# Kernel tuning notes

Hardware: AMD Instinct MI355X
Metric: run time of the kernel (lower is better)

Reference implementation:

```python
import jax, jax.numpy as jnp
import numpy as np
import math

B, N, H, NH, HD, G = 2, 1024, 512, 8, 64, 50
MAX_DIST = 10.0


def setup_inputs() -> dict:
    key = jax.random.key(0)
    ks = jax.random.split(key, 12)
    s = 0.02  # small init scale for weights
    return {
        'x': jax.random.normal(ks[0], (B, N, H), jnp.float32),
        'distances': jax.random.uniform(ks[1], (B, N, N), jnp.float32) * MAX_DIST,
        'mask': jnp.ones((B, N), jnp.int32),
        'widths': jnp.ones((G,), jnp.float32) * 0.5,
        'dp_w': jax.random.normal(ks[2], (G, NH), jnp.float32) * s,
        'dp_b': jnp.zeros((NH,), jnp.float32),
        'wq': jax.random.normal(ks[3], (H, H), jnp.float32) * s,
        'bq': jnp.zeros((H,), jnp.float32),
        'wk': jax.random.normal(ks[4], (H, H), jnp.float32) * s,
        'bk': jnp.zeros((H,), jnp.float32),
        'wv': jax.random.normal(ks[5], (H, H), jnp.float32) * s,
        'bv': jnp.zeros((H,), jnp.float32),
        'wo': jax.random.normal(ks[6], (H, H), jnp.float32) * s,
        'bo': jnp.zeros((H,), jnp.float32),
        'ln1_g': jnp.ones((H,), jnp.float32),
        'ln1_b': jnp.zeros((H,), jnp.float32),
        'ln2_g': jnp.ones((H,), jnp.float32),
        'ln2_b': jnp.zeros((H,), jnp.float32),
        'w1': jax.random.normal(ks[7], (H, 4 * H), jnp.float32) * s,
        'b1': jnp.zeros((4 * H,), jnp.float32),
        'w2': jax.random.normal(ks[8], (4 * H, H), jnp.float32) * s,
        'b2': jnp.zeros((H,), jnp.float32),
    }


def _layernorm(x, g, b, eps=1e-5):
    mu = jnp.mean(x, axis=-1, keepdims=True)
    var = jnp.mean(jnp.square(x - mu), axis=-1, keepdims=True)
    return (x - mu) * jax.lax.rsqrt(var + eps) * g + b


def reference(x, distances, mask, widths, dp_w, dp_b, wq, bq, wk, bk, wv, bv,
              wo, bo, ln1_g, ln1_b, ln2_g, ln2_b, w1, b1, w2, b2):
    centers = jnp.linspace(0.0, MAX_DIST, G, dtype=jnp.float32)  # buffer

    residual = x
    xn = _layernorm(x, ln1_g, ln1_b)

    def split_heads(t):  # [B,N,H] -> [B,NH,N,HD]
        return t.reshape(B, N, NH, HD).transpose(0, 2, 1, 3)

    q = split_heads(xn @ wq + bq)
    k = split_heads(xn @ wk + bk)
    v = split_heads(xn @ wv + bv)

    scores = jnp.einsum('bhqd,bhkd->bhqk', q, k) / math.sqrt(HD)

    # Gaussian distance encoding: [B,N,N,G]
    diff = distances[..., None] - centers
    gf = jnp.exp(-jnp.square(diff) / (2.0 * jnp.square(widths)))
    # project to per-head bias, then permute to [B,NH,N,N]
    dist_bias = (gf @ dp_w + dp_b).transpose(0, 3, 1, 2)
    scores = scores + dist_bias

    key_mask = mask[:, None, None, :]  # [B,1,1,N]
    scores = jnp.where(key_mask == 0, -1e9, scores)

    attn = jax.nn.softmax(scores, axis=-1)
    out = jnp.einsum('bhqk,bhkd->bhqd', attn, v)
    out = out.transpose(0, 2, 1, 3).reshape(B, N, H)
    out = out @ wo + bo

    x = residual + out
    residual = x
    xn = _layernorm(x, ln2_g, ln2_b)
    h = jax.nn.gelu(xn @ w1 + b1, approximate=False)  # dropout is identity in eval
    x = residual + (h @ w2 + b2)
    return x
```

## Files before the change

### kernel.cpp

```cpp
#include <hip/hip_runtime.h>
#include <hip/hip_bf16.h>
#include <math.h>

#define B_ 2
#define N_ 1024
#define H_ 512
#define NH_ 8
#define HD_ 64
#define G_ 50
#define TAB_ 1024
constexpr float MAXD = 10.0f;

typedef __attribute__((ext_vector_type(8))) short short8;
typedef __attribute__((ext_vector_type(4))) float f32x4;

__device__ inline ushort f2bf(float v) {
  __hip_bfloat16 h = __float2bfloat16(v);
  return *(ushort*)&h;
}
__device__ inline float bf2f(ushort u) {
  unsigned x = ((unsigned)u) << 16;
  return __uint_as_float(x);
}
__device__ inline void gload_lds16(const ushort* g, ushort* l) {
  __builtin_amdgcn_global_load_lds(
      (const __attribute__((address_space(1))) void*)g,
      (__attribute__((address_space(3))) void*)l, 16, 0, 0);
}

__device__ inline void transp_dev(const float* __restrict__ src,
                                  ushort* __restrict__ d, int R, int C,
                                  int bx, int by, int t, float (*tile)[33]) {
  int r0 = by * 32, c0 = bx * 32;
  int rr = t >> 5, cc = t & 31;
  #pragma unroll
  for (int p = 0; p < 4; ++p)
    tile[rr + p * 8][cc] = src[(size_t)(r0 + rr + p * 8) * C + c0 + cc];
  __syncthreads();
  #pragma unroll
  for (int p = 0; p < 4; ++p)
    d[(size_t)(c0 + rr + p * 8) * R + r0 + cc] = f2bf(tile[cc][rr + p * 8]);
}

__global__ __launch_bounds__(256) void prep_k(
    const float* wq, const float* wk, const float* wv, const float* wo,
    const float* w1, const float* w2, ushort* __restrict__ wT4,
    ushort* __restrict__ w1T, ushort* __restrict__ w2T,
    const float* __restrict__ widths, const float* __restrict__ dp_w,
    const float* __restrict__ dp_b, float2* __restrict__ tab2,
    const float* __restrict__ x, const float* __restrict__ ln1g,
    const float* __restrict__ ln1b, ushort* __restrict__ xn) {
  __shared__ float tile[32][33];
  __shared__ float red2[4][2];
  int bid = blockIdx.x, t = threadIdx.x;
  if (bid < 1024) {
    int z = bid >> 8, rem = bid & 255;
    const float* src = (z == 0) ? wq : (z == 1) ? wk : (z == 2) ? wv : wo;
    transp_dev(src, wT4 + (size_t)z * 512 * 512, 512, 512, rem & 15, rem >> 4, t, tile);
  } else if (bid < 2048) {
    int rem = bid - 1024;
    transp_dev(w1, w1T, 512, 2048, rem & 63, rem >> 6, t, tile);
  } else if (bid < 3072) {
    int rem = bid - 2048;
    transp_dev(w2, w2T, 2048, 512, rem & 15, rem >> 4, t, tile);
  } else if (bid < 3105) {
    int i = (bid - 3072) * 256 + t;
    if (i >= NH_ * (TAB_ + 1)) return;
    int h = i / (TAB_ + 1), tt = i % (TAB_ + 1);
    int t1 = tt < TAB_ ? tt + 1 : tt;
    float d0 = (float)tt * (MAXD / TAB_);
    float d1 = (float)t1 * (MAXD / TAB_);
    float v0 = dp_b[h], v1 = dp_b[h];
    for (int g = 0; g < G_; ++g) {
      float c = (float)g * (MAXD / 49.0f);
      float w = widths[g];
      float inv = -1.0f / (2.0f * w * w);
      float wg = dp_w[g * NH_ + h];
      float e0 = d0 - c, e1 = d1 - c;
      v0 += expf(e0 * e0 * inv) * wg;
      v1 += expf(e1 * e1 * inv) * wg;
    }
    tab2[i] = make_float2(v0, v1);
  } else {
    int row = (bid - 3105) * 2 + (t >> 7);
    int tl = t & 127;
    float4 v = *(const float4*)(x + (size_t)row * H_ + tl * 4);
    float s = v.x + v.y + v.z + v.w;
    float sq = v.x * v.x + v.y * v.y + v.z * v.z + v.w * v.w;
    #pragma unroll
    for (int m = 1; m < 64; m <<= 1) {
      s += __shfl_xor(s, m, 64);
      sq += __shfl_xor(sq, m, 64);
    }
    int wid = t >> 6;
    if ((t & 63) == 0) { red2[wid][0] = s; red2[wid][1] = sq; }
    __syncthreads();
    int rw = (t >> 7) * 2;
    s = red2[rw][0] + red2[rw + 1][0];
    sq = red2[rw][1] + red2[rw + 1][1];
    float mu = s * (1.0f / H_);
    float var = sq * (1.0f / H_) - mu * mu;
    float rs = rsqrtf(var + 1e-5f);
    float4 gg = *(const float4*)(ln1g + tl * 4);
    float4 bb = *(const float4*)(ln1b + tl * 4);
    ushort4 o;
    o.x = f2bf((v.x - mu) * rs * gg.x + bb.x);
    o.y = f2bf((v.y - mu) * rs * gg.y + bb.y);
    o.z = f2bf((v.z - mu) * rs * gg.z + bb.z);
    o.w = f2bf((v.w - mu) * rs * gg.w + bb.w);
    *(ushort4*)(xn + (size_t)row * H_ + tl * 4) = o;
  }
}

enum { EPI_QKV = 1, EPI_RES = 2, EPI_GELU = 3, EPI_PART = 4 };

template <int BM, int BN, int EPI>
__global__ __launch_bounds__(256) void mfma_gemm(const ushort* __restrict__ A,
                                                 const ushort* __restrict__ Bt,
                                                 const float* __restrict__ b0,
                                                 const float* __restrict__ b1,
                                                 const float* __restrict__ b2,
                                                 const float* __restrict__ resid,
                                                 void* __restrict__ outv,
                                                 int K, int Ks, int Nc) {
  __shared__ ushort As[2][BM * 32];
  __shared__ ushort Bs[2][BN * 32];
  int t = threadIdx.x;
  int z = blockIdx.z;
  const ushort* Bz;
  int k0;
  if constexpr (EPI == EPI_PART) {
    Bz = Bt;
    k0 = z * K;
  } else {
    Bz = Bt + (size_t)z * Nc * Ks;
    k0 = 0;
  }
  const float* bias = (z == 0) ? b0 : (z == 1) ? b1 : b2;
  int m0 = blockIdx.y * BM, n0 = blockIdx.x * BN;
  int lane = t & 63, w = t >> 6, wr = w >> 1, wc = w & 1;
  int lrow = lane & 15, lkg = lane >> 4;
  constexpr int NFM = BM / 32, NFN = BN / 32;
  constexpr int AL = BM / 64, BL = BN / 64;
  f32x4 acc[NFM][NFN] = {};
  int rl = lane >> 2, kgl = lane & 3;

  auto stage = [&](int buf, int kt) {
    #pragma unroll
    for (int p = 0; p < AL; ++p) {
      int r = w * (BM / 4) + p * 16 + rl;
      int kgs = kgl ^ (r & 3);
      gload_lds16(&A[(size_t)(m0 + r) * Ks + k0 + kt + kgs * 8],
                  &As[buf][(w * (BM / 4) + p * 16) * 32]);
    }
    #pragma unroll
    for (int p = 0; p < BL; ++p) {
      int r = w * (BN / 4) + p * 16 + rl;
      int kgs = kgl ^ (r & 3);
      gload_lds16(&Bz[(size_t)(n0 + r) * Ks + k0 + kt + kgs * 8],
                  &Bs[buf][(w * (BN / 4) + p * 16) * 32]);
    }
  };
  auto compute = [&](int buf) {
    short8 af[NFM], bfr[NFN];
    #pragma unroll
    for (int fm = 0; fm < NFM; ++fm) {
      int r = wr * (BM / 2) + fm * 16 + lrow;
      af[fm] = *(const short8*)&As[buf][r * 32 + ((lkg ^ (r & 3)) << 3)];
    }
    #pragma unroll
    for (int fn = 0; fn < NFN; ++fn) {
      int r = wc * (BN / 2) + fn * 16 + lrow;
      bfr[fn] = *(const short8*)&Bs[buf][r * 32 + ((lkg ^ (r & 3)) << 3)];
    }
    #pragma unroll
    for (int fm = 0; fm < NFM; ++fm)
      #pragma unroll
      for (int fn = 0; fn < NFN; ++fn)
        acc[fm][fn] = __builtin_amdgcn_mfma_f32_16x16x32_bf16(af[fm], bfr[fn],
                                                              acc[fm][fn], 0, 0, 0);
  };

  stage(0, 0);
  __syncthreads();
  int cur = 0;
  for (int kt = 0; kt < K; kt += 32) {
    if (kt + 32 < K) stage(cur ^ 1, kt + 32);
    compute(cur);
    __syncthreads();
    cur ^= 1;
  }

  int rbase = (lane >> 4) * 4;
  #pragma unroll
  for (int fm = 0; fm < NFM; ++fm) {
    #pragma unroll
    for (int fn = 0; fn < NFN; ++fn) {
      #pragma unroll
      for (int j = 0; j < 4; ++j) {
        int row = m0 + wr * (BM / 2) + fm * 16 + rbase + j;
        int col = n0 + wc * (BN / 2) + fn * 16 + lrow;
        if constexpr (EPI == EPI_PART) {
          size_t M = (size_t)gridDim.y * BM;
          ((float*)outv)[(size_t)z * M * Nc + (size_t)row * Nc + col] =
              acc[fm][fn][j];
        } else {
          float v = acc[fm][fn][j] + bias[col];
          if constexpr (EPI == EPI_QKV) {
            ushort* q = (ushort*)outv + (size_t)z * (1 << 20);
            int bb = row >> 10, n = row & (N_ - 1);
            int h = col >> 6, d = col & 63;
            if (z < 2)
              q[(((size_t)(bb * NH_ + h)) * N_ + n) * HD_ + d] = f2bf(v);
            else
              q[(((size_t)(bb * NH_ + h)) * HD_ + d) * N_ + n] = f2bf(v);
          } else if constexpr (EPI == EPI_RES) {
            ((float*)outv)[(size_t)row * Nc + col] =
                resid[(size_t)row * Nc + col] + v;
          } else {
            ((ushort*)outv)[(size_t)row * Nc + col] =
                f2bf(0.5f * v * (1.0f + erff(v * 0.70710678118654752f)));
          }
        }
      }
    }
  }
}

__global__ __launch_bounds__(256) void comb2_k(const float* __restrict__ p,
                                               const float* __restrict__ resid,
                                               const float* __restrict__ bias,
                                               float* __restrict__ out) {
  int idx = blockIdx.x * 256 + threadIdx.x;
  int base = idx * 4;
  int col = base & (H_ - 1);
  f32x4 a = *(const f32x4*)&p[base];
  f32x4 b = *(const f32x4*)&p[(1 << 20) + base];
  f32x4 r = *(const f32x4*)&resid[base];
  f32x4 bi = *(const f32x4*)&bias[col];
  f32x4 o = r + a + b + bi;
  *(f32x4*)&out[base] = o;
}

__global__ __launch_bounds__(128) void comb2ln_k(const float* __restrict__ p,
                                                 const float* __restrict__ resid,
                                                 const float* __restrict__ bias,
                                                 const float* __restrict__ g,
                                                 const float* __restrict__ bl,
                                                 float* __restrict__ x1out,
                                                 ushort* __restrict__ xnout) {
  int row = blockIdx.x, t = threadIdx.x;
  int base = row * H_ + t * 4;
  f32x4 a = *(const f32x4*)&p[base];
  f32x4 b2v = *(const f32x4*)&p[(1 << 20) + base];
  f32x4 r = *(const f32x4*)&resid[base];
  f32x4 bi = *(const f32x4*)&bias[t * 4];
  f32x4 v = r + a + b2v + bi;
  *(f32x4*)&x1out[base] = v;
  float s = v[0] + v[1] + v[2] + v[3];
  float sq = v[0] * v[0] + v[1] * v[1] + v[2] * v[2] + v[3] * v[3];
  #pragma unroll
  for (int m = 1; m < 64; m <<= 1) {
    s += __shfl_xor(s, m, 64);
    sq += __shfl_xor(sq, m, 64);
  }
  __shared__ float red[2][2];
  int wid = t >> 6;
  if ((t & 63) == 0) { red[wid][0] = s; red[wid][1] = sq; }
  __syncthreads();
  s = red[0][0] + red[1][0];
  sq = red[0][1] + red[1][1];
  float mu = s * (1.0f / H_);
  float var = sq * (1.0f / H_) - mu * mu;
  float rs = rsqrtf(var + 1e-5f);
  float4 gg = *(const float4*)(g + t * 4);
  float4 bb = *(const float4*)(bl + t * 4);
  ushort4 o;
  o.x = f2bf((v[0] - mu) * rs * gg.x + bb.x);
  o.y = f2bf((v[1] - mu) * rs * gg.y + bb.y);
  o.z = f2bf((v[2] - mu) * rs * gg.z + bb.z);
  o.w = f2bf((v[3] - mu) * rs * gg.w + bb.w);
  *(ushort4*)(xnout + (size_t)row * H_ + t * 4) = o;
}

constexpr int QT = 64, KT = 64, NJH = 2, NTH = N_ / (KT * NJH);
constexpr int JH = N_ / NJH;

__global__ __launch_bounds__(256) void attn_k(
    const ushort* __restrict__ q, const ushort* __restrict__ k,
    const ushort* __restrict__ v, const float* __restrict__ dist,
    const int* __restrict__ mask, const float2* __restrict__ tab2g,
    float* __restrict__ Op, float2* __restrict__ ml) {
  int qt = blockIdx.x, h = blockIdx.y, z = blockIdx.z;
  int b = z >> 1, jh = z & 1;
  int i0 = qt * QT;
  int jbase = jh * JH;
  __shared__ ushort Ks[2][KT * 64];
  __shared__ ushort Vt[2][64 * KT];
  __shared__ ushort Bsb[2][QT * 68];
  __shared__ ushort Ps[4][16 * 64];
  __shared__ float2 tl2[TAB_ + 1];
  __shared__ float mfl[JH];
  int t = threadIdx.x;
  int lane = t & 63, w = t >> 6;
  int l = lane & 15, g = lane >> 4;

  for (int i = t; i <= TAB_; i += 256) tl2[i] = tab2g[h * (TAB_ + 1) + i];
  for (int i = t; i < JH; i += 256) mfl[i] = (mask[b * N_ + jbase + i] == 0) ? -1e9f : 0.0f;

  const size_t ho = ((size_t)(b * NH_ + h)) * N_ * HD_;
  const ushort* qb = q + ho;
  const ushort* kb = k + ho;
  const ushort* vb = v + ho;

  int qrow = i0 + w * 16 + l;
  short8 qf[2];
  qf[0] = *(const short8*)&qb[(size_t)qrow * 64 + g * 8];
  qf[1] = *(const short8*)&qb[(size_t)qrow * 64 + 32 + g * 8];

  int c2 = t & 7, jr = t >> 3;
  int dr_r = t >> 2, dr_c = (t & 3) * 16;

  auto stK = [&](int buf, short8 val, int j2) {
    *(short8*)&Ks[buf][j2 * 64 + ((c2 ^ (j2 & 7)) << 3)] = val;
  };
  auto stV = [&](int buf, short8 val, int d) {
    *(short8*)&Vt[buf][d * 64 + ((c2 ^ (d & 7)) << 3)] = val;
  };

  short8 k0a, k1a, v0a, v1a;
  f32x4 dda[4];
  {
    const ushort* kn = kb + (size_t)jbase * 64;
    const ushort* vn = vb + jbase;
    k0a = *(const short8*)&kn[(size_t)jr * 64 + c2 * 8];
    k1a = *(const short8*)&kn[(size_t)(jr + 32) * 64 + c2 * 8];
    v0a = *(const short8*)&vn[(size_t)jr * N_ + c2 * 8];
    v1a = *(const short8*)&vn[(size_t)(jr + 32) * N_ + c2 * 8];
    const float* db = dist + ((size_t)b * N_ + (i0 + dr_r)) * N_ + jbase + dr_c;
    #pragma unroll
    for (int p = 0; p < 4; ++p) dda[p] = *(const f32x4*)&db[p * 4];
  }
  __syncthreads();
  {
    stK(0, k0a, jr); stK(0, k1a, jr + 32);
    stV(0, v0a, jr); stV(0, v1a, jr + 32);
    #pragma unroll
    for (int p = 0; p < 4; ++p) {
      ushort4 ov;
      #pragma unroll
      for (int e = 0; e < 4; ++e) {
        int jcol = dr_c + p * 4 + e;
        float u = dda[p][e] * ((float)TAB_ / MAXD);
        int it = (int)u;
        it = it < 0 ? 0 : (it > TAB_ - 1 ? TAB_ - 1 : it);
        float f = u - (float)it;
        float2 tv = tl2[it];
        ((ushort*)&ov)[e] = f2bf(tv.x + f * (tv.y - tv.x) + mfl[jcol]);
      }
      *(ushort4*)&Bsb[0][dr_r * 68 + dr_c + p * 4] = ov;
    }
  }
  __syncthreads();

  float m_[4] = {-1e30f, -1e30f, -1e30f, -1e30f};
  float l_[4] = {0.f, 0.f, 0.f, 0.f};
  f32x4 acc[4] = {{0,0,0,0},{0,0,0,0},{0,0,0,0},{0,0,0,0}};

  int cur = 0;
  for (int tt = 0; tt < NTH; ++tt) {
    const int j0 = jbase + tt * KT;
    if (tt + 1 < NTH) {
      const ushort* kn = kb + (size_t)(j0 + KT) * 64;
      const ushort* vn = vb + (j0 + KT);
      k0a = *(const short8*)&kn[(size_t)jr * 64 + c2 * 8];
      k1a = *(const short8*)&kn[(size_t)(jr + 32) * 64 + c2 * 8];
      v0a = *(const short8*)&vn[(size_t)jr * N_ + c2 * 8];
      v1a = *(const short8*)&vn[(size_t)(jr + 32) * N_ + c2 * 8];
      const float* db = dist + ((size_t)b * N_ + (i0 + dr_r)) * N_ + j0 + KT + dr_c;
      #pragma unroll
      for (int p = 0; p < 4; ++p) dda[p] = *(const f32x4*)&db[p * 4];
    }
    f32x4 sa[4] = {{0,0,0,0},{0,0,0,0},{0,0,0,0},{0,0,0,0}};
    __builtin_amdgcn_s_setprio(1);
    #pragma unroll
    for (int dblk = 0; dblk < 2; ++dblk)
      #pragma unroll
      for (int fj = 0; fj < 4; ++fj) {
        int j2 = fj * 16 + l;
        short8 kf = *(const short8*)&Ks[cur][j2 * 64 + (((dblk * 4 + g) ^ (j2 & 7)) << 3)];
        sa[fj] = __builtin_amdgcn_mfma_f32_16x16x32_bf16(qf[dblk], kf, sa[fj], 0, 0, 0);
      }
    __builtin_amdgcn_s_setprio(0);
    float al_[4];
    int qloc = w * 16 + 4 * g;
    #pragma unroll
    for (int reg = 0; reg < 4; ++reg) {
      float svr[4];
      #pragma unroll
      for (int fj = 0; fj < 4; ++fj)
        svr[fj] = fmaf(sa[fj][reg], 0.125f,
                       bf2f(Bsb[cur][(qloc + reg) * 68 + fj * 16 + l]));
      float rm = fmaxf(fmaxf(svr[0], svr[1]), fmaxf(svr[2], svr[3]));
      rm = fmaxf(rm, __shfl_xor(rm, 1, 64));
      rm = fmaxf(rm, __shfl_xor(rm, 2, 64));
      rm = fmaxf(rm, __shfl_xor(rm, 4, 64));
      rm = fmaxf(rm, __shfl_xor(rm, 8, 64));
      float mn = fmaxf(m_[reg], rm);
      float al = __expf(m_[reg] - mn);
      m_[reg] = mn;
      al_[reg] = al;
      float ps = 0.f;
      int qlq = 4 * g + reg;
      #pragma unroll
      for (int fj = 0; fj < 4; ++fj) {
        float p = __expf(svr[fj] - mn);
        ps += p;
        int c = fj * 2 + (l >> 3);
        Ps[w][qlq * 64 + ((c ^ (qlq & 7)) << 3) + (l & 7)] = f2bf(p);
      }
      ps += __shfl_xor(ps, 1, 64);
      ps += __shfl_xor(ps, 2, 64);
      ps += __shfl_xor(ps, 4, 64);
      ps += __shfl_xor(ps, 8, 64);
      l_[reg] = l_[reg] * al + ps;
    }
    #pragma unroll
    for (int fd = 0; fd < 4; ++fd)
      #pragma unroll
      for (int reg = 0; reg < 4; ++reg) acc[fd][reg] *= al_[reg];
    __builtin_amdgcn_s_setprio(1);
    #pragma unroll
    for (int jj = 0; jj < 2; ++jj) {
      short8 pa = *(const short8*)&Ps[w][l * 64 + (((jj * 4 + g) ^ (l & 7)) << 3)];
      #pragma unroll
      for (int fd = 0; fd < 4; ++fd) {
        int d2 = fd * 16 + l;
        short8 vf = *(const short8*)&Vt[cur][d2 * 64 + (((jj * 4 + g) ^ (d2 & 7)) << 3)];
        acc[fd] = __builtin_amdgcn_mfma_f32_16x16x32_bf16(pa, vf, acc[fd], 0, 0, 0);
      }
    }
    __builtin_amdgcn_s_setprio(0);
    if (tt + 1 < NTH) {
      int nb = cur ^ 1;
      stK(nb, k0a, jr); stK(nb, k1a, jr + 32);
      stV(nb, v0a, jr); stV(nb, v1a, jr + 32);
      const int jloc = (tt + 1) * KT;
      #pragma unroll
      for (int p = 0; p < 4; ++p) {
        ushort4 ov;
        #pragma unroll
        for (int e = 0; e < 4; ++e) {
          int jcol = dr_c + p * 4 + e;
          float u = dda[p][e] * ((float)TAB_ / MAXD);
          int it = (int)u;
          it = it < 0 ? 0 : (it > TAB_ - 1 ? TAB_ - 1 : it);
          float f = u - (float)it;
          float2 tv = tl2[it];
          ((ushort*)&ov)[e] = f2bf(tv.x + f * (tv.y - tv.x) + mfl[jloc + jcol]);
        }
        *(ushort4*)&Bsb[nb][dr_r * 68 + dr_c + p * 4] = ov;
      }
    }
    __syncthreads();
    cur ^= 1;
  }
  const size_t pbase = (((size_t)(b * NJH + jh) * NH_ + h) * N_) + i0;
  #pragma unroll
  for (int reg = 0; reg < 4; ++reg) {
    int rowl = w * 16 + 4 * g + reg;
    float* op = Op + (pbase + rowl) * HD_ + l;
    #pragma unroll
    for (int fd = 0; fd < 4; ++fd) op[fd * 16] = acc[fd][reg];
    if (l == 0) ml[pbase + rowl] = make_float2(m_[reg], l_[reg]);
  }
}

__global__ __launch_bounds__(256) void comb_k(const float* __restrict__ Op,
                                              const float2* __restrict__ ml,
                                              ushort* __restrict__ ao) {
  int idx = blockIdx.x * 256 + threadIdx.x;
  int row = idx >> 4;
  int dq = (idx & 15) * 4;
  int b = row >> 13, h = (row >> 10) & 7, n = row & 1023;
  size_t p0 = (((size_t)(b * NJH + 0) * NH_ + h) * N_) + n;
  size_t p1 = (((size_t)(b * NJH + 1) * NH_ + h) * N_) + n;
  float2 v0 = ml[p0], v1 = ml[p1];
  float M = fmaxf(v0.x, v1.x);
  float a0 = __expf(v0.x - M), a1 = __expf(v1.x - M);
  float inv = 1.0f / (v0.y * a0 + v1.y * a1);
  float4 O0 = *(const float4*)&Op[p0 * HD_ + dq];
  float4 O1 = *(const float4*)&Op[p1 * HD_ + dq];
  ushort4 o;
  o.x = f2bf((O0.x * a0 + O1.x * a1) * inv);
  o.y = f2bf((O0.y * a0 + O1.y * a1) * inv);
  o.z = f2bf((O0.z * a0 + O1.z * a1) * inv);
  o.w = f2bf((O0.w * a0 + O1.w * a1) * inv);
  *(ushort4*)&ao[((size_t)(b * N_ + n)) * H_ + h * HD_ + dq] = o;
}

extern "C" void kernel_launch(void* const* d_in, const int* in_sizes, int n_in,
                              void* d_out, int out_size, void* d_ws, size_t ws_size,
                              hipStream_t stream) {
  const float* x = (const float*)d_in[0];
  const float* distances = (const float*)d_in[1];
  const int* mask = (const int*)d_in[2];
  const float* widths = (const float*)d_in[3];
  const float* dp_w = (const float*)d_in[4];
  const float* dp_b = (const float*)d_in[5];
  const float* wq = (const float*)d_in[6];
  const float* bq = (const float*)d_in[7];
  const float* wk = (const float*)d_in[8];
  const float* bk = (const float*)d_in[9];
  const float* wv = (const float*)d_in[10];
  const float* bv = (const float*)d_in[11];
  const float* wo = (const float*)d_in[12];
  const float* bo = (const float*)d_in[13];
  const float* ln1_g = (const float*)d_in[14];
  const float* ln1_b = (const float*)d_in[15];
  const float* ln2_g = (const float*)d_in[16];
  const float* ln2_b = (const float*)d_in[17];
  const float* w1 = (const float*)d_in[18];
  const float* b1 = (const float*)d_in[19];
  const float* w2 = (const float*)d_in[20];
  const float* b2 = (const float*)d_in[21];
  float* out = (float*)d_out;
  float* wsf = (float*)d_ws;

  const size_t M1 = (size_t)1 << 20;
  ushort* qkvb = (ushort*)wsf;
  float* x1 = wsf + 2 * M1;
  ushort* hbuf = (ushort*)(wsf + 3 * M1);
  ushort* xn = (ushort*)(wsf + 5 * M1);
  ushort* xn2 = (ushort*)(wsf + 5 * M1 + M1 / 2);
  ushort* ao = (ushort*)(wsf + 6 * M1);
  ushort* wT4 = (ushort*)(wsf + 6 * M1 + M1 / 2);
  ushort* w1T = (ushort*)(wsf + 7 * M1);
  ushort* w2T = (ushort*)(wsf + 7 * M1 + M1 / 2);
  float2* tab2 = (float2*)(wsf + 8 * M1);
  float* Op = wsf + 9 * M1;
  float2* ml = (float2*)(wsf + 11 * M1);
  float* pAO = wsf + 12 * M1;
  float* pF2 = wsf + 14 * M1;

  prep_k<<<4129, 256, 0, stream>>>(wq, wk, wv, wo, w1, w2, wT4, w1T, w2T,
                                   widths, dp_w, dp_b, tab2, x, ln1_g, ln1_b, xn);

  mfma_gemm<64, 64, EPI_QKV><<<dim3(8, 32, 3), 256, 0, stream>>>(
      xn, wT4, bq, bk, bv, nullptr, qkvb, 512, 512, 512);

  attn_k<<<dim3(N_ / QT, NH_, B_ * NJH), 256, 0, stream>>>(
      qkvb, qkvb + M1, qkvb + 2 * M1, distances, mask, tab2, Op, ml);
  comb_k<<<1024, 256, 0, stream>>>(Op, ml, ao);

  mfma_gemm<64, 64, EPI_PART><<<dim3(8, 32, 2), 256, 0, stream>>>(
      ao, wT4 + (size_t)3 * 512 * 512, bo, bo, bo, nullptr, pAO, 256, 512, 512);
  comb2ln_k<<<B_ * N_, 128, 0, stream>>>(pAO, x, bo, ln2_g, ln2_b, x1, xn2);

  mfma_gemm<128, 64, EPI_GELU><<<dim3(32, 16, 1), 256, 0, stream>>>(
      xn2, w1T, b1, b1, b1, nullptr, hbuf, 512, 512, 2048);

  mfma_gemm<64, 64, EPI_PART><<<dim3(8, 32, 2), 256, 0, stream>>>(
      hbuf, w2T, b2, b2, b2, nullptr, pF2, 1024, 2048, 512);
  comb2_k<<<1024, 256, 0, stream>>>(pF2, x1, b2, out);
}
```

Measured before the change: 103.5 us.

## Reduce split-K partials inside a 512-thread block and fuse FFN2 residual epilogue

```diff
diff --git a/kernel.cpp b/kernel.cpp
--- a/kernel.cpp
+++ b/kernel.cpp
@@ -127,15 +127,7 @@
   __shared__ ushort Bs[2][BN * 32];
   int t = threadIdx.x;
   int z = blockIdx.z;
-  const ushort* Bz;
-  int k0;
-  if constexpr (EPI == EPI_PART) {
-    Bz = Bt;
-    k0 = z * K;
-  } else {
-    Bz = Bt + (size_t)z * Nc * Ks;
-    k0 = 0;
-  }
+  const ushort* Bz = Bt + (size_t)z * Nc * Ks;
   const float* bias = (z == 0) ? b0 : (z == 1) ? b1 : b2;
   int m0 = blockIdx.y * BM, n0 = blockIdx.x * BN;
   int lane = t & 63, w = t >> 6, wr = w >> 1, wc = w & 1;
@@ -150,14 +142,14 @@
     for (int p = 0; p < AL; ++p) {
       int r = w * (BM / 4) + p * 16 + rl;
       int kgs = kgl ^ (r & 3);
-      gload_lds16(&A[(size_t)(m0 + r) * Ks + k0 + kt + kgs * 8],
+      gload_lds16(&A[(size_t)(m0 + r) * Ks + kt + kgs * 8],
                   &As[buf][(w * (BM / 4) + p * 16) * 32]);
     }
     #pragma unroll
     for (int p = 0; p < BL; ++p) {
       int r = w * (BN / 4) + p * 16 + rl;
       int kgs = kgl ^ (r & 3);
-      gload_lds16(&Bz[(size_t)(n0 + r) * Ks + k0 + kt + kgs * 8],
+      gload_lds16(&Bz[(size_t)(n0 + r) * Ks + kt + kgs * 8],
                   &Bs[buf][(w * (BN / 4) + p * 16) * 32]);
     }
   };
@@ -200,46 +192,119 @@
       for (int j = 0; j < 4; ++j) {
         int row = m0 + wr * (BM / 2) + fm * 16 + rbase + j;
         int col = n0 + wc * (BN / 2) + fn * 16 + lrow;
-        if constexpr (EPI == EPI_PART) {
-          size_t M = (size_t)gridDim.y * BM;
-          ((float*)outv)[(size_t)z * M * Nc + (size_t)row * Nc + col] =
-              acc[fm][fn][j];
+        float v = acc[fm][fn][j] + bias[col];
+        if constexpr (EPI == EPI_QKV) {
+          ushort* q = (ushort*)outv + (size_t)z * (1 << 20);
+          int bb = row >> 10, n = row & (N_ - 1);
+          int h = col >> 6, d = col & 63;
+          if (z < 2)
+            q[(((size_t)(bb * NH_ + h)) * N_ + n) * HD_ + d] = f2bf(v);
+          else
+            q[(((size_t)(bb * NH_ + h)) * HD_ + d) * N_ + n] = f2bf(v);
+        } else if constexpr (EPI == EPI_RES) {
+          ((float*)outv)[(size_t)row * Nc + col] =
+              resid[(size_t)row * Nc + col] + v;
         } else {
-          float v = acc[fm][fn][j] + bias[col];
-          if constexpr (EPI == EPI_QKV) {
-            ushort* q = (ushort*)outv + (size_t)z * (1 << 20);
-            int bb = row >> 10, n = row & (N_ - 1);
-            int h = col >> 6, d = col & 63;
-            if (z < 2)
-              q[(((size_t)(bb * NH_ + h)) * N_ + n) * HD_ + d] = f2bf(v);
-            else
-              q[(((size_t)(bb * NH_ + h)) * HD_ + d) * N_ + n] = f2bf(v);
-          } else if constexpr (EPI == EPI_RES) {
+          ((ushort*)outv)[(size_t)row * Nc + col] =
+              f2bf(0.5f * v * (1.0f + erff(v * 0.70710678118654752f)));
+        }
+      }
+    }
+  }
+}
+
+template <int EPI>
+__global__ __launch_bounds__(512) void mfma_gemm2(const ushort* __restrict__ A,
+                                                  const ushort* __restrict__ Bt,
+                                                  const float* __restrict__ bias,
+                                                  const float* __restrict__ resid,
+                                                  void* __restrict__ outv,
+                                                  int K, int Ks, int Nc) {
+  constexpr int BM = 64, BN = 64;
+  __shared__ ushort AsBs[2][2][2][BM * 32];
+  int t = threadIdx.x;
+  int half = t >> 8;
+  int lane = t & 63;
+  int wl = (t >> 6) & 3;
+  int wr = wl >> 1, wc = wl & 1;
+  int lrow = lane & 15, lkg = lane >> 4;
+  int k0 = half * K;
+  int m0 = blockIdx.y * BM, n0 = blockIdx.x * BN;
+  f32x4 acc[2][2] = {};
+  int rl = lane >> 2, kgl = lane & 3;
+
+  auto stage = [&](int buf, int kt) {
+    int r = wl * 16 + rl;
+    int kgs = kgl ^ (r & 3);
+    gload_lds16(&A[(size_t)(m0 + r) * Ks + k0 + kt + kgs * 8],
+                &AsBs[0][half][buf][(wl * 16) * 32]);
+    gload_lds16(&Bt[(size_t)(n0 + r) * Ks + k0 + kt + kgs * 8],
+                &AsBs[1][half][buf][(wl * 16) * 32]);
+  };
+  auto compute = [&](int buf) {
+    short8 af[2], bfr[2];
+    #pragma unroll
+    for (int fm = 0; fm < 2; ++fm) {
+      int r = wr * 32 + fm * 16 + lrow;
+      af[fm] = *(const short8*)&AsBs[0][half][buf][r * 32 + ((lkg ^ (r & 3)) << 3)];
+    }
+    #pragma unroll
+    for (int fn = 0; fn < 2; ++fn) {
+      int r = wc * 32 + fn * 16 + lrow;
+      bfr[fn] = *(const short8*)&AsBs[1][half][buf][r * 32 + ((lkg ^ (r & 3)) << 3)];
+    }
+    #pragma unroll
+    for (int fm = 0; fm < 2; ++fm)
+      #pragma unroll
+      for (int fn = 0; fn < 2; ++fn)
+        acc[fm][fn] = __builtin_amdgcn_mfma_f32_16x16x32_bf16(af[fm], bfr[fn],
+                                                              acc[fm][fn], 0, 0, 0);
+  };
+
+  stage(0, 0);
+  __syncthreads();
+  int cur = 0;
+  for (int kt = 0; kt < K; kt += 32) {
+    if (kt + 32 < K) stage(cur ^ 1, kt + 32);
+    compute(cur);
+    __syncthreads();
+    cur ^= 1;
+  }
+
+  float* red = (float*)&AsBs[0][0][0][0];
+  int rbase = (lane >> 4) * 4;
+  if (half == 1) {
+    #pragma unroll
+    for (int fm = 0; fm < 2; ++fm)
+      #pragma unroll
+      for (int fn = 0; fn < 2; ++fn)
+        #pragma unroll
+        for (int j = 0; j < 4; ++j) {
+          int rloc = wr * 32 + fm * 16 + rbase + j;
+          int cloc = wc * 32 + fn * 16 + lrow;
+          red[rloc * 65 + cloc] = acc[fm][fn][j];
+        }
+  }
+  __syncthreads();
+  if (half == 0) {
+    #pragma unroll
+    for (int fm = 0; fm < 2; ++fm)
+      #pragma unroll
+      for (int fn = 0; fn < 2; ++fn)
+        #pragma unroll
+        for (int j = 0; j < 4; ++j) {
+          int rloc = wr * 32 + fm * 16 + rbase + j;
+          int cloc = wc * 32 + fn * 16 + lrow;
+          float sum = acc[fm][fn][j] + red[rloc * 65 + cloc];
+          int row = m0 + rloc, col = n0 + cloc;
+          if constexpr (EPI == EPI_PART) {
+            ((float*)outv)[(size_t)row * Nc + col] = sum;
+          } else {
             ((float*)outv)[(size_t)row * Nc + col] =
-                resid[(size_t)row * Nc + col] + v;
-          } else {
-            ((ushort*)outv)[(size_t)row * Nc + col] =
-                f2bf(0.5f * v * (1.0f + erff(v * 0.70710678118654752f)));
+                resid[(size_t)row * Nc + col] + sum + bias[col];
           }
         }
-      }
-    }
-  }
-}
-
-__global__ __launch_bounds__(256) void comb2_k(const float* __restrict__ p,
-                                               const float* __restrict__ resid,
-                                               const float* __restrict__ bias,
-                                               float* __restrict__ out) {
-  int idx = blockIdx.x * 256 + threadIdx.x;
-  int base = idx * 4;
-  int col = base & (H_ - 1);
-  f32x4 a = *(const f32x4*)&p[base];
-  f32x4 b = *(const f32x4*)&p[(1 << 20) + base];
-  f32x4 r = *(const f32x4*)&resid[base];
-  f32x4 bi = *(const f32x4*)&bias[col];
-  f32x4 o = r + a + b + bi;
-  *(f32x4*)&out[base] = o;
+  }
 }
 
 __global__ __launch_bounds__(128) void comb2ln_k(const float* __restrict__ p,
@@ -252,10 +317,9 @@
   int row = blockIdx.x, t = threadIdx.x;
   int base = row * H_ + t * 4;
   f32x4 a = *(const f32x4*)&p[base];
-  f32x4 b2v = *(const f32x4*)&p[(1 << 20) + base];
   f32x4 r = *(const f32x4*)&resid[base];
   f32x4 bi = *(const f32x4*)&bias[t * 4];
-  f32x4 v = r + a + b2v + bi;
+  f32x4 v = r + a + bi;
   *(f32x4*)&x1out[base] = v;
   float s = v[0] + v[1] + v[2] + v[3];
   float sq = v[0] * v[0] + v[1] * v[1] + v[2] * v[2] + v[3] * v[3];
@@ -541,7 +605,6 @@
   float* Op = wsf + 9 * M1;
   float2* ml = (float2*)(wsf + 11 * M1);
   float* pAO = wsf + 12 * M1;
-  float* pF2 = wsf + 14 * M1;
 
   prep_k<<<4129, 256, 0, stream>>>(wq, wk, wv, wo, w1, w2, wT4, w1T, w2T,
                                    widths, dp_w, dp_b, tab2, x, ln1_g, ln1_b, xn);
@@ -553,14 +616,13 @@
       qkvb, qkvb + M1, qkvb + 2 * M1, distances, mask, tab2, Op, ml);
   comb_k<<<1024, 256, 0, stream>>>(Op, ml, ao);
 
-  mfma_gemm<64, 64, EPI_PART><<<dim3(8, 32, 2), 256, 0, stream>>>(
-      ao, wT4 + (size_t)3 * 512 * 512, bo, bo, bo, nullptr, pAO, 256, 512, 512);
+  mfma_gemm2<EPI_PART><<<dim3(8, 32), 512, 0, stream>>>(
+      ao, wT4 + (size_t)3 * 512 * 512, bo, nullptr, pAO, 256, 512, 512);
   comb2ln_k<<<B_ * N_, 128, 0, stream>>>(pAO, x, bo, ln2_g, ln2_b, x1, xn2);
 
   mfma_gemm<128, 64, EPI_GELU><<<dim3(32, 16, 1), 256, 0, stream>>>(
       xn2, w1T, b1, b1, b1, nullptr, hbuf, 512, 512, 2048);
 
-  mfma_gemm<64, 64, EPI_PART><<<dim3(8, 32, 2), 256, 0, stream>>>(
-      hbuf, w2T, b2, b2, b2, nullptr, pF2, 1024, 2048, 512);
-  comb2_k<<<1024, 256, 0, stream>>>(pF2, x1, b2, out);
-}
+  mfma_gemm2<EPI_RES><<<dim3(8, 32), 512, 0, stream>>>(
+      hbuf, w2T, b2, x1, out, 1024, 2048, 512);
+}
```

New measurement: 98.81 us. -4.5%, faster.
